# Performance work log

Hardware: AMD Instinct MI355X
Metric: run time of the kernel (lower is better)

## Reference

```python
import jax, jax.numpy as jnp
import numpy as np

N = 2048


def setup_inputs() -> dict:
    key = jax.random.key(0)
    k1, k2 = jax.random.split(key)
    graph1 = jax.random.uniform(k1, (N, N), dtype=jnp.float32)
    graph2 = jax.random.uniform(k2, (N, N), dtype=jnp.float32)
    return {"graph1": graph1, "graph2": graph2}


def _degree_dist(adj):
    return adj.sum(axis=-1)


def _clustering(adj):
    # diag(A @ A @ A) computed without materializing the full cube:
    # tri_i = sum_j (A@A)_{ij} * A_{ji}
    a2 = adj @ adj                      # [n, n]
    tri = (a2 * adj.T).sum(axis=-1)     # [n]
    deg = adj.sum(axis=-1)
    deg = jnp.where(deg < 2, 1.0, deg)  # torch: deg[deg < 2] = 1
    return tri / (deg * (deg - 1.0))


def reference(graph1, graph2):
    d1 = _degree_dist(graph1)
    d2 = _degree_dist(graph2)
    degree_sim = jnp.exp(-jnp.abs(d1 - d2).mean())
    c1 = _clustering(graph1)
    c2 = _clustering(graph2)
    cluster_sim = jnp.exp(-jnp.abs(c1 - c2).mean())
    overall = (degree_sim + cluster_sim) / 2.0
    return (degree_sim, cluster_sim, overall)
```

## Files before the change

### kernel.cpp

```cpp
#include <hip/hip_runtime.h>

#define NN 2048

typedef unsigned short u16;
typedef unsigned char u8;
typedef __attribute__((ext_vector_type(4))) float floatx4;

__device__ __forceinline__ float fp8_to_f32(unsigned v) {
  const unsigned e = (v >> 3) & 15, m = v & 7;
  const float norm = __uint_as_float(((e + 120u) << 23) | (m << 20));
  const float sub = (float)m * 0.001953125f;
  return e == 0 ? sub : norm;
}

__device__ __forceinline__ void load_lds16(const u8* g, u8* l) {
  __builtin_amdgcn_global_load_lds(
      (const __attribute__((address_space(1))) unsigned int*)g,
      (__attribute__((address_space(3))) unsigned int*)l,
      16, 0, 0);
}

__global__ __launch_bounds__(256) void prep_kernel(
    const float* __restrict__ A1, const float* __restrict__ A2,
    u8* __restrict__ A8, u8* __restrict__ A8T,
    float* __restrict__ degp, float* __restrict__ tri) {
  __shared__ unsigned Tl[64 * 17];
  const int bx = blockIdx.x, by = blockIdx.y, bz = blockIdx.z;
  const float* __restrict__ A = bz ? A2 : A1;
  u8* __restrict__ ab = A8 + (size_t)bz * (NN * (size_t)NN);
  u8* __restrict__ at = A8T + (size_t)bz * (NN * (size_t)NN);
  float* __restrict__ dp = degp + (size_t)bz * (32 * NN);
  const int t = threadIdx.x;
  const int r0 = by * 64, c0 = bx * 64;
  const int q = t >> 4, cs = t & 15;

  if (bx == 0 && t < 64) tri[bz * NN + by * 64 + t] = 0.f;

  unsigned rowpack[4];
#pragma unroll
  for (int d = 0; d < 4; ++d) {
    const int r = 4 * q + d;
    const float4 fv = *(const float4*)(A + (size_t)(r0 + r) * NN + c0 + cs * 4);
    int pk = __builtin_amdgcn_cvt_pk_fp8_f32(fv.x, fv.y, 0, false);
    pk = __builtin_amdgcn_cvt_pk_fp8_f32(fv.z, fv.w, pk, true);
    rowpack[d] = (unsigned)pk;
    *(unsigned*)(ab + (size_t)(r0 + r) * NN + c0 + cs * 4) = (unsigned)pk;
    float s = fv.x + fv.y + fv.z + fv.w;
    s += __shfl_xor(s, 1); s += __shfl_xor(s, 2);
    s += __shfl_xor(s, 4); s += __shfl_xor(s, 8);
    if (cs == 0) dp[(size_t)(r0 + r) * 32 + bx] = s;
  }
#pragma unroll
  for (int e = 0; e < 4; ++e) {
    const unsigned tc = ((rowpack[0] >> (8 * e)) & 0xFFu) |
                        (((rowpack[1] >> (8 * e)) & 0xFFu) << 8) |
                        (((rowpack[2] >> (8 * e)) & 0xFFu) << 16) |
                        (((rowpack[3] >> (8 * e)) & 0xFFu) << 24);
    Tl[(4 * cs + e) * 17 + q] = tc;
  }
  __syncthreads();
#pragma unroll
  for (int p = 0; p < 2; ++p) {
    const int rp = p * 32 + (t >> 3);
    const int mm = t & 7;
    uint2 v;
    v.x = Tl[rp * 17 + 2 * mm];
    v.y = Tl[rp * 17 + 2 * mm + 1];
    *(uint2*)(at + (size_t)(c0 + rp) * NN + r0 + mm * 8) = v;
  }
}

#define MFMA_BODY(PB)                                                      \
  {                                                                        \
    long aL[4][2], bL[4][2];                                               \
    _Pragma("unroll")                                                      \
    for (int tm = 0; tm < 4; ++tm) {                                       \
      aL[tm][0] = *(const long*)(smem + (PB) + aoff[tm][0]);               \
      aL[tm][1] = *(const long*)(smem + (PB) + aoff[tm][1]);               \
    }                                                                      \
    _Pragma("unroll")                                                      \
    for (int tn = 0; tn < 4; ++tn) {                                       \
      bL[tn][0] = *(const long*)(smem + (PB) + boff[tn][0]);               \
      bL[tn][1] = *(const long*)(smem + (PB) + boff[tn][1]);               \
    }                                                                      \
    _Pragma("unroll")                                                      \
    for (int tm = 0; tm < 4; ++tm)                                         \
      _Pragma("unroll")                                                    \
      for (int tn = 0; tn < 4; ++tn) {                                     \
        acc[tm][tn] = __builtin_amdgcn_mfma_f32_16x16x32_fp8_fp8(          \
            aL[tm][0], bL[tn][0], acc[tm][tn], 0, 0, 0);                   \
        acc[tm][tn] = __builtin_amdgcn_mfma_f32_16x16x32_fp8_fp8(          \
            aL[tm][1], bL[tn][1], acc[tm][tn], 0, 0, 0);                   \
      }                                                                    \
  }

#define PREFETCH(KK, DB)                                                   \
  load_lds16(gA0 + (KK), smem + (DB) + sA0);                               \
  load_lds16(gA1 + (KK), smem + (DB) + sA1);                               \
  load_lds16(gB0 + (KK), smem + (DB) + sB0);                               \
  load_lds16(gB1 + (KK), smem + (DB) + sB1);

#define FENCE asm volatile("" ::: "memory")

__global__ __launch_bounds__(256, 4) void gemm_tri_kernel(
    const u8* __restrict__ A8, const u8* __restrict__ A8T,
    float* __restrict__ tri) {
  __shared__ __align__(16) u8 smem[32768];

  const int tid = threadIdx.x;
  const int w = tid >> 6, lane = tid & 63;
  const int wm = w >> 1, wn = w & 1;
  const int cl = lane & 15, g = lane >> 4;
  const int i0 = blockIdx.y * 128, j0 = blockIdx.x * 128;
  const int mz = blockIdx.z >> 1, kz = blockIdx.z & 1;
  const size_t mat = (size_t)mz * (NN * (size_t)NN);
  const u8* __restrict__ Am = A8 + mat;
  const u8* __restrict__ ATm = A8T + mat;
  float* __restrict__ triM = tri + mz * NN;

  const int s0 = (w * 2 + 0) * 64 + lane;
  const int s1 = (w * 2 + 1) * 64 + lane;
  const int r0s = s0 >> 2, c0s = (s0 & 3) ^ ((r0s >> 1) & 3);
  const int r1s = s1 >> 2, c1s = (s1 & 3) ^ ((r1s >> 1) & 3);
  const int kbase = kz * 1024;
  const u8* gA0 = Am + (size_t)(i0 + r0s) * NN + kbase + c0s * 16;
  const u8* gA1 = Am + (size_t)(i0 + r1s) * NN + kbase + c1s * 16;
  const u8* gB0 = ATm + (size_t)(j0 + r0s) * NN + kbase + c0s * 16;
  const u8* gB1 = ATm + (size_t)(j0 + r1s) * NN + kbase + c1s * 16;
  const int sA0 = (w * 2 + 0) * 1024, sA1 = (w * 2 + 1) * 1024;
  const int sB0 = 8192 + sA0, sB1 = 8192 + sA1;

  const int rsw = (cl >> 1) & 3;
  const int sub = (g & 1) * 8, ch = g >> 1;
  int aoff[4][2], boff[4][2];
#pragma unroll
  for (int tm = 0; tm < 4; ++tm) {
    const int r = wm * 64 + tm * 16 + cl;
#pragma unroll
    for (int h = 0; h < 2; ++h)
      aoff[tm][h] = r * 64 + (((2 * h + ch) ^ rsw) * 16) + sub;
  }
#pragma unroll
  for (int tn = 0; tn < 4; ++tn) {
    const int r = wn * 64 + tn * 16 + cl;
#pragma unroll
    for (int h = 0; h < 2; ++h)
      boff[tn][h] = 8192 + r * 64 + (((2 * h + ch) ^ rsw) * 16) + sub;
  }

  floatx4 acc[4][4] = {};

  PREFETCH(0, 0)

#pragma unroll 1
  for (int d = 0; d < 7; ++d) {
    FENCE; __builtin_amdgcn_s_barrier(); FENCE;
    PREFETCH((2 * d + 1) * 64, 16384)
    __builtin_amdgcn_s_waitcnt(0x0F74);
    FENCE; __builtin_amdgcn_s_barrier(); FENCE;
    MFMA_BODY(0)
    FENCE; __builtin_amdgcn_s_barrier(); FENCE;
    PREFETCH((2 * d + 2) * 64, 0)
    __builtin_amdgcn_s_waitcnt(0x0F74);
    FENCE; __builtin_amdgcn_s_barrier(); FENCE;
    MFMA_BODY(16384)
  }
  FENCE; __builtin_amdgcn_s_barrier(); FENCE;
  PREFETCH(15 * 64, 16384)
  __builtin_amdgcn_s_waitcnt(0x0F74);
  FENCE; __builtin_amdgcn_s_barrier(); FENCE;
  MFMA_BODY(0)
  FENCE; __builtin_amdgcn_s_barrier(); FENCE;
  __builtin_amdgcn_s_waitcnt(0x0F70);
  FENCE; __builtin_amdgcn_s_barrier(); FENCE;
  MFMA_BODY(16384)

  __syncthreads();
#pragma unroll
  for (int it = 0; it < 4; ++it) {
    const int idx = tid + it * 256;
    const int r = idx >> 3, co = (idx & 7) * 16;
    *(uint4*)(smem + r * 144 + co) =
        *(const uint4*)(ATm + (size_t)(i0 + r) * NN + j0 + co);
  }
  __syncthreads();

#pragma unroll
  for (int tm = 0; tm < 4; ++tm) {
#pragma unroll
    for (int reg = 0; reg < 4; ++reg) {
      const int rloc = wm * 64 + tm * 16 + g * 4 + reg;
      float v = 0.f;
#pragma unroll
      for (int tn = 0; tn < 4; ++tn) {
        const int cloc = wn * 64 + tn * 16 + cl;
        v += acc[tm][tn][reg] * fp8_to_f32(smem[rloc * 144 + cloc]);
      }
      v += __shfl_xor(v, 1);
      v += __shfl_xor(v, 2);
      v += __shfl_xor(v, 4);
      v += __shfl_xor(v, 8);
      if (cl == 0) atomicAdd(&triM[i0 + rloc], v);
    }
  }
}

__global__ __launch_bounds__(1024) void finalize1_kernel(
    const float* __restrict__ degp, const float* __restrict__ tri,
    float* __restrict__ part) {
  __shared__ float red[32];
  const int t = threadIdx.x;
  const int r = blockIdx.x * 128 + (t >> 3);
  const int q = (t & 7) * 4;
  const float4 v1 = *(const float4*)(degp + (size_t)r * 32 + q);
  const float4 v2 = *(const float4*)(degp + 32 * NN + (size_t)r * 32 + q);
  float d1 = v1.x + v1.y + v1.z + v1.w;
  float d2 = v2.x + v2.y + v2.z + v2.w;
#pragma unroll
  for (int m = 1; m < 8; m <<= 1) {
    d1 += __shfl_xor(d1, m);
    d2 += __shfl_xor(d2, m);
  }
  float sdd = 0.f, scc = 0.f;
  if ((t & 7) == 0) {
    const float t1 = tri[r], t2 = tri[NN + r];
    const float e1 = d1 < 2.f ? 1.f : d1;
    const float e2 = d2 < 2.f ? 1.f : d2;
    sdd = fabsf(d1 - d2);
    scc = fabsf(t1 / (e1 * (e1 - 1.f)) - t2 / (e2 * (e2 - 1.f)));
  }
#pragma unroll
  for (int m = 8; m < 64; m <<= 1) {
    sdd += __shfl_xor(sdd, m);
    scc += __shfl_xor(scc, m);
  }
  const int wv = t >> 6, ln = t & 63;
  if (ln == 0) { red[wv] = sdd; red[16 + wv] = scc; }
  __syncthreads();
  if (t == 0) {
    float a = 0.f, b = 0.f;
#pragma unroll
    for (int i = 0; i < 16; ++i) { a += red[i]; b += red[16 + i]; }
    part[blockIdx.x * 2 + 0] = a;
    part[blockIdx.x * 2 + 1] = b;
  }
}

__global__ void finalize2_kernel(const float* __restrict__ part,
                                 float* __restrict__ out) {
  if (threadIdx.x == 0) {
    float a = 0.f, b = 0.f;
#pragma unroll
    for (int i = 0; i < 16; ++i) { a += part[i * 2]; b += part[i * 2 + 1]; }
    const float ds = expf(-a * (1.f / (float)NN));
    const float cs = expf(-b * (1.f / (float)NN));
    out[0] = ds;
    out[1] = cs;
    out[2] = 0.5f * (ds + cs);
  }
}

extern "C" void kernel_launch(void* const* d_in, const int* in_sizes, int n_in,
                              void* d_out, int out_size, void* d_ws, size_t ws_size,
                              hipStream_t stream) {
  (void)in_sizes; (void)n_in; (void)out_size; (void)ws_size;
  const float* A1 = (const float*)d_in[0];
  const float* A2 = (const float*)d_in[1];
  float* out = (float*)d_out;

  u8* A8 = (u8*)d_ws;
  u8* A8T = A8 + 2 * (size_t)NN * NN;
  float* tri = (float*)(A8T + 2 * (size_t)NN * NN);
  float* degp = tri + 2 * NN;
  float* part = degp + 2 * 32 * NN;

  prep_kernel<<<dim3(32, 32, 2), 256, 0, stream>>>(A1, A2, A8, A8T, degp, tri);
  gemm_tri_kernel<<<dim3(16, 16, 4), 256, 0, stream>>>(A8, A8T, tri);
  finalize1_kernel<<<16, 1024, 0, stream>>>(degp, tri, part);
  finalize2_kernel<<<1, 64, 0, stream>>>(part, out);
}
```

Measured before the change: 115.9 us.

## Fuse finalize kernels into GEMM via last-block reduction and remap block order

Removes the two finalize kernel launches by having the last GEMM block, found with an atomic counter, compute the degree/clustering reductions and the outputs. The counter is reset in prep_kernel. It also remaps the block index so consecutive blocks are spread across matrix/k-split slices, which changes which tiles are resident on XCDs at the same time. The tail reduction now runs on a single 256-thread block, and every block pays a threadfence and an atomic.

```diff
diff --git a/kernel.cpp b/kernel.cpp
--- a/kernel.cpp
+++ b/kernel.cpp
@@ -23,7 +23,8 @@
 __global__ __launch_bounds__(256) void prep_kernel(
     const float* __restrict__ A1, const float* __restrict__ A2,
     u8* __restrict__ A8, u8* __restrict__ A8T,
-    float* __restrict__ degp, float* __restrict__ tri) {
+    float* __restrict__ degp, float* __restrict__ tri,
+    unsigned* __restrict__ cnt) {
   __shared__ unsigned Tl[64 * 17];
   const int bx = blockIdx.x, by = blockIdx.y, bz = blockIdx.z;
   const float* __restrict__ A = bz ? A2 : A1;
@@ -35,6 +36,7 @@
   const int q = t >> 4, cs = t & 15;
 
   if (bx == 0 && t < 64) tri[bz * NN + by * 64 + t] = 0.f;
+  if (bx == 0 && by == 0 && bz == 0 && t == 0) cnt[0] = 0u;
 
   unsigned rowpack[4];
 #pragma unroll
@@ -104,15 +106,21 @@
 
 __global__ __launch_bounds__(256, 4) void gemm_tri_kernel(
     const u8* __restrict__ A8, const u8* __restrict__ A8T,
-    float* __restrict__ tri) {
+    float* __restrict__ tri, const float* __restrict__ degp,
+    float* __restrict__ out, unsigned* __restrict__ cnt) {
   __shared__ __align__(16) u8 smem[32768];
 
   const int tid = threadIdx.x;
   const int w = tid >> 6, lane = tid & 63;
   const int wm = w >> 1, wn = w & 1;
   const int cl = lane & 15, g = lane >> 4;
-  const int i0 = blockIdx.y * 128, j0 = blockIdx.x * 128;
-  const int mz = blockIdx.z >> 1, kz = blockIdx.z & 1;
+
+  const int L = blockIdx.x + (blockIdx.y << 4) + (blockIdx.z << 8);
+  const int nl = (L & 7) * 128 + (L >> 3);
+  const int bx = nl & 15, by = (nl >> 4) & 15, bz = nl >> 8;
+
+  const int i0 = by * 128, j0 = bx * 128;
+  const int mz = bz >> 1, kz = bz & 1;
   const size_t mat = (size_t)mz * (NN * (size_t)NN);
   const u8* __restrict__ Am = A8 + mat;
   const u8* __restrict__ ATm = A8T + mat;
@@ -203,55 +211,42 @@
       if (cl == 0) atomicAdd(&triM[i0 + rloc], v);
     }
   }
-}
-
-__global__ __launch_bounds__(1024) void finalize1_kernel(
-    const float* __restrict__ degp, const float* __restrict__ tri,
-    float* __restrict__ part) {
-  __shared__ float red[32];
-  const int t = threadIdx.x;
-  const int r = blockIdx.x * 128 + (t >> 3);
-  const int q = (t & 7) * 4;
-  const float4 v1 = *(const float4*)(degp + (size_t)r * 32 + q);
-  const float4 v2 = *(const float4*)(degp + 32 * NN + (size_t)r * 32 + q);
-  float d1 = v1.x + v1.y + v1.z + v1.w;
-  float d2 = v2.x + v2.y + v2.z + v2.w;
-#pragma unroll
-  for (int m = 1; m < 8; m <<= 1) {
-    d1 += __shfl_xor(d1, m);
-    d2 += __shfl_xor(d2, m);
-  }
+
+  __threadfence();
+  __shared__ int isLast;
+  if (tid == 0) isLast = (atomicAdd(cnt, 1u) == (16 * 16 * 4 - 1));
+  __syncthreads();
+  if (!isLast) return;
+  __threadfence();
+
   float sdd = 0.f, scc = 0.f;
-  if ((t & 7) == 0) {
-    const float t1 = tri[r], t2 = tri[NN + r];
+  for (int rr = tid; rr < NN; rr += 256) {
+    const float4* p1 = (const float4*)(degp + (size_t)rr * 32);
+    const float4* p2 = (const float4*)(degp + 32 * (size_t)NN + (size_t)rr * 32);
+    float d1 = 0.f, d2 = 0.f;
+#pragma unroll
+    for (int qq = 0; qq < 8; ++qq) {
+      const float4 v1 = p1[qq], v2 = p2[qq];
+      d1 += v1.x + v1.y + v1.z + v1.w;
+      d2 += v2.x + v2.y + v2.z + v2.w;
+    }
+    const float t1 = tri[rr], t2 = tri[NN + rr];
     const float e1 = d1 < 2.f ? 1.f : d1;
     const float e2 = d2 < 2.f ? 1.f : d2;
-    sdd = fabsf(d1 - d2);
-    scc = fabsf(t1 / (e1 * (e1 - 1.f)) - t2 / (e2 * (e2 - 1.f)));
-  }
-#pragma unroll
-  for (int m = 8; m < 64; m <<= 1) {
+    sdd += fabsf(d1 - d2);
+    scc += fabsf(t1 / (e1 * (e1 - 1.f)) - t2 / (e2 * (e2 - 1.f)));
+  }
+#pragma unroll
+  for (int m = 1; m < 64; m <<= 1) {
     sdd += __shfl_xor(sdd, m);
     scc += __shfl_xor(scc, m);
   }
-  const int wv = t >> 6, ln = t & 63;
-  if (ln == 0) { red[wv] = sdd; red[16 + wv] = scc; }
-  __syncthreads();
-  if (t == 0) {
-    float a = 0.f, b = 0.f;
-#pragma unroll
-    for (int i = 0; i < 16; ++i) { a += red[i]; b += red[16 + i]; }
-    part[blockIdx.x * 2 + 0] = a;
-    part[blockIdx.x * 2 + 1] = b;
-  }
-}
-
-__global__ void finalize2_kernel(const float* __restrict__ part,
-                                 float* __restrict__ out) {
-  if (threadIdx.x == 0) {
-    float a = 0.f, b = 0.f;
-#pragma unroll
-    for (int i = 0; i < 16; ++i) { a += part[i * 2]; b += part[i * 2 + 1]; }
+  __shared__ float redf[8];
+  if (lane == 0) { redf[w] = sdd; redf[4 + w] = scc; }
+  __syncthreads();
+  if (tid == 0) {
+    const float a = redf[0] + redf[1] + redf[2] + redf[3];
+    const float b = redf[4] + redf[5] + redf[6] + redf[7];
     const float ds = expf(-a * (1.f / (float)NN));
     const float cs = expf(-b * (1.f / (float)NN));
     out[0] = ds;
@@ -272,10 +267,10 @@
   u8* A8T = A8 + 2 * (size_t)NN * NN;
   float* tri = (float*)(A8T + 2 * (size_t)NN * NN);
   float* degp = tri + 2 * NN;
-  float* part = degp + 2 * 32 * NN;
-
-  prep_kernel<<<dim3(32, 32, 2), 256, 0, stream>>>(A1, A2, A8, A8T, degp, tri);
-  gemm_tri_kernel<<<dim3(16, 16, 4), 256, 0, stream>>>(A8, A8T, tri);
-  finalize1_kernel<<<16, 1024, 0, stream>>>(degp, tri, part);
-  finalize2_kernel<<<1, 64, 0, stream>>>(part, out);
-}
+  unsigned* cnt = (unsigned*)(degp + 2 * 32 * NN);
+
+  prep_kernel<<<dim3(32, 32, 2), 256, 0, stream>>>(A1, A2, A8, A8T, degp, tri,
+                                                   cnt);
+  gemm_tri_kernel<<<dim3(16, 16, 4), 256, 0, stream>>>(A8, A8T, tri, degp, out,
+                                                       cnt);
+}
```

Result: slower. 208.9 us (+80.2%).
